# Optimization experiments

Hardware: AMD Instinct MI355X
Metric: run time of the kernel (lower is better)

Reference implementation:

```python
import jax, jax.numpy as jnp
import numpy as np

B, T, V, K = 4, 1024, 32000, 50000
EPS_T, EPS_M = 1e-8, 1e-12


def setup_inputs() -> dict:
    key = jax.random.key(0)
    k1, k2, k3, k4 = jax.random.split(key, 4)
    probs = jax.random.uniform(k1, (B, T, V), dtype=jnp.float32)
    # normalize so rows are valid distributions (faithful to softmax outputs)
    probs = probs / probs.sum(-1, keepdims=True)
    target_probs = jax.random.uniform(k2, (K,), dtype=jnp.float32) * (1.0 / K)
    target_oov = jax.random.uniform(k3, (1,), dtype=jnp.float32)
    mask = jnp.ones((B, T), dtype=bool)
    pairs = jax.random.randint(k4, (K, 2), 0, V, dtype=jnp.int64 if jax.config.jax_enable_x64 else jnp.int32)
    return {"probs": probs, "target_probs": target_probs, "target_oov": target_oov,
            "mask": mask, "pairs": pairs}


def reference(probs, target_probs, target_oov, mask, pairs):
    a = pairs[:, 0]  # (K,)
    b = pairs[:, 1]
    p_t = probs[:, :-1, :]   # (B, T-1, V)
    p_t1 = probs[:, 1:, :]
    pair_mask = (mask[:, :-1] & mask[:, 1:]).astype(jnp.float32)  # (B, T-1)
    # gather bigram probs: (B, T-1, K) joint, masked sum over batch/seq
    joint = p_t[..., a] * p_t1[..., b]
    topk_sum = jnp.einsum('btk,bt->k', joint, pair_mask)  # (K,)
    n_pairs = pair_mask.sum()

    # finalize
    n = jnp.maximum(n_pairs, 1.0)
    model_top = jnp.maximum(topk_sum / n, EPS_M)
    model_oov = jnp.clip(1.0 - model_top.sum(), EPS_M, 1.0 - EPS_T)
    tgt = jnp.maximum(target_probs, EPS_T)
    t_oov = jnp.maximum(target_oov[0], EPS_T)
    kl_top = (model_top * (jnp.log(model_top) - jnp.log(tgt))).sum()
    kl_oov = model_oov * (jnp.log(model_oov) - jnp.log(t_oov))
    return kl_top + kl_oov
```

## Files before the change

### kernel.cpp

```cpp
#include <hip/hip_runtime.h>
#include <stdint.h>

#define B_   4
#define T_   1024
#define V_   32000
#define K_   50000
#define N_   (B_*(T_-1))
#define TPB  1024
#define U_   49
#define KP   (TPB*U_)
#define POS_PER_BLK 16
#define G1   ((N_ + POS_PER_BLK - 1)/POS_PER_BLK)
#define EPSTGT 1e-8f
#define EPSMOD 1e-12f
#define MAXSLOTS 64

__device__ __forceinline__ uint32_t bf16rne(float x) {
    uint32_t u = __float_as_uint(x);
    u += 0x7FFFu + ((u >> 16) & 1u);
    return u >> 16;
}

__device__ __forceinline__ void stage_row(const float* __restrict__ probs, int r,
                                          ushort* dst, int tid) {
    const float4* src = (const float4*)(probs + (size_t)r * V_);
    for (int i = tid; i < V_ / 4; i += TPB) {
        float4 v = src[i];
        uint2 pk;
        pk.x = bf16rne(v.x) | (bf16rne(v.y) << 16);
        pk.y = bf16rne(v.z) | (bf16rne(v.w) << 16);
        *(uint2*)(dst + i * 4) = pk;
    }
}

__global__ void k_pack(const int* __restrict__ pairs, uint32_t* __restrict__ ppk) {
    int k = blockIdx.x * 256 + threadIdx.x;
    if (k >= KP) return;
    uint32_t v = 0;
    if (k < K_) {
        uint32_t a = (uint32_t)pairs[2 * k];
        uint32_t b = (uint32_t)pairs[2 * k + 1];
        v = ((a * 2u) << 16) | (b * 2u);
    }
    ppk[k] = v;
}

__global__ void k_mask(const unsigned char* __restrict__ mask, float* __restrict__ scalars) {
    __shared__ int red[16];
    int tid = threadIdx.x;
    int cnt = 0;
    for (int n = tid; n < N_; n += 1024) {
        int b = n / (T_ - 1);
        int t = n - b * (T_ - 1);
        int r = b * T_ + t;
        cnt += (mask[r] && mask[r + 1]) ? 1 : 0;
    }
    for (int off = 32; off > 0; off >>= 1) cnt += __shfl_down(cnt, off, 64);
    int wid = tid >> 6, lid = tid & 63;
    if (lid == 0) red[wid] = cnt;
    __syncthreads();
    if (tid == 0) {
        int s = 0;
        for (int w = 0; w < 16; ++w) s += red[w];
        scalars[0] = (float)s;
    }
}

__global__ __launch_bounds__(TPB) void k_main(
    const float* __restrict__ probs,
    const unsigned char* __restrict__ mask,
    const uint32_t* __restrict__ ppk,
    float* __restrict__ partials, int S)
{
    __shared__ __align__(16) ushort rows[2][V_];
    const int tid = threadIdx.x;
    const int g = blockIdx.x;
    const int n0 = g * POS_PER_BLK;
    const int n1 = min(N_, n0 + POS_PER_BLK);

    float acc[U_];
#pragma unroll
    for (int u = 0; u < U_; ++u) acc[u] = 0.f;

    int staged = -1;
    for (int n = n0; n < n1; ++n) {
        const int b = n / (T_ - 1);
        const int t = n - b * (T_ - 1);
        const int r0 = b * T_ + t;
        const int r1 = r0 + 1;

        __syncthreads();
        if (staged != r0) stage_row(probs, r0, rows[r0 & 1], tid);
        stage_row(probs, r1, rows[r1 & 1], tid);
        staged = r1;
        __syncthreads();

        if (!(mask[r0] && mask[r1])) continue;

        const ushort* rp = rows[r0 & 1];
        const ushort* rq = rows[r1 & 1];
        const uint32_t* pp = ppk + tid;
#pragma unroll
        for (int c = 0; c < U_; c += 7) {
            uint32_t pk[7];
#pragma unroll
            for (int j = 0; j < 7; ++j) pk[j] = pp[(c + j) * TPB];
#pragma unroll
            for (int j = 0; j < 7; ++j) {
                uint32_t ao = pk[j] >> 16;
                uint32_t bo = pk[j] & 0xFFFFu;
                ushort av = *(const ushort*)((const char*)rp + ao);
                ushort bv = *(const ushort*)((const char*)rq + bo);
                float af = __uint_as_float(((uint32_t)av) << 16);
                float bf = __uint_as_float(((uint32_t)bv) << 16);
                acc[c + j] = fmaf(af, bf, acc[c + j]);
            }
        }
    }

    float* slot = partials + (size_t)(g % S) * KP;
#pragma unroll
    for (int u = 0; u < U_; ++u)
        atomicAdd(slot + u * TPB + tid, acc[u]);
}

__global__ void k_reduce(const float* __restrict__ partials, const float* __restrict__ tgt,
                         float* __restrict__ scalars, int S) {
    int k = blockIdx.x * 256 + threadIdx.x;
    float n = fmaxf(scalars[0], 1.0f);
    float mt = 0.f, term = 0.f;
    if (k < K_) {
        float ts = 0.f;
        for (int s = 0; s < S; ++s) ts += partials[(size_t)s * KP + k];
        mt = fmaxf(ts / n, EPSMOD);
        float tg = fmaxf(tgt[k], EPSTGT);
        term = mt * (__logf(mt) - __logf(tg));
    }
    for (int off = 32; off > 0; off >>= 1) {
        mt += __shfl_down(mt, off, 64);
        term += __shfl_down(term, off, 64);
    }
    __shared__ float rm[4], rt[4];
    int wid = threadIdx.x >> 6, lid = threadIdx.x & 63;
    if (lid == 0) { rm[wid] = mt; rt[wid] = term; }
    __syncthreads();
    if (threadIdx.x == 0) {
        float sm = 0.f, st = 0.f;
        for (int w = 0; w < 4; ++w) { sm += rm[w]; st += rt[w]; }
        atomicAdd(&scalars[1], sm);
        atomicAdd(&scalars[2], st);
    }
}

__global__ void k_final(const float* __restrict__ scalars, const float* __restrict__ toov,
                        float* __restrict__ out) {
    float S1 = scalars[1], S2 = scalars[2];
    float moov = 1.f - S1;
    moov = fminf(fmaxf(moov, EPSMOD), 1.f - EPSTGT);
    float tv = fmaxf(toov[0], EPSTGT);
    out[0] = S2 + moov * (__logf(moov) - __logf(tv));
}

extern "C" void kernel_launch(void* const* d_in, const int* in_sizes, int n_in,
                              void* d_out, int out_size, void* d_ws, size_t ws_size,
                              hipStream_t stream) {
    const float* probs = (const float*)d_in[0];
    const float* tgt   = (const float*)d_in[1];
    const float* toov  = (const float*)d_in[2];
    const unsigned char* mask = (const unsigned char*)d_in[3];
    const int* pairs   = (const int*)d_in[4];
    float* out = (float*)d_out;

    char* ws = (char*)d_ws;
    uint32_t* ppk = (uint32_t*)ws;
    size_t off_sc = (size_t)KP * 4;
    float* scalars = (float*)(ws + off_sc);
    size_t off_pt = off_sc + 256;
    float* partials = (float*)(ws + off_pt);

    long avail = (long)ws_size - (long)off_pt;
    int S = (int)(avail / ((long)KP * 4));
    if (S > MAXSLOTS) S = MAXSLOTS;
    if (S < 1) S = 1;

    hipMemsetAsync(ws + off_sc, 0, 256 + (size_t)S * KP * 4, stream);
    k_pack<<<(KP + 255) / 256, 256, 0, stream>>>(pairs, ppk);
    k_mask<<<1, 1024, 0, stream>>>(mask, scalars);
    k_main<<<G1, TPB, 0, stream>>>(probs, mask, ppk, partials, S);
    k_reduce<<<(K_ + 255) / 256, 256, 0, stream>>>(partials, tgt, scalars, S);
    k_final<<<1, 1, 0, stream>>>(scalars, toov, out);
}
```

Before: 751.4 us.

## Prefetch next probability row into registers while computing current bigram gathers

Result: no change. 747.7 us (-0.5%).

```diff
diff --git a/kernel.cpp b/kernel.cpp
--- a/kernel.cpp
+++ b/kernel.cpp
@@ -14,22 +14,25 @@
 #define EPSTGT 1e-8f
 #define EPSMOD 1e-12f
 #define MAXSLOTS 64
+#define W4   (V_/4)
 
 __device__ __forceinline__ uint32_t bf16rne(float x) {
     uint32_t u = __float_as_uint(x);
     u += 0x7FFFu + ((u >> 16) & 1u);
     return u >> 16;
 }
+__device__ __forceinline__ uint2 pack4(float4 v) {
+    uint2 pk;
+    pk.x = bf16rne(v.x) | (bf16rne(v.y) << 16);
+    pk.y = bf16rne(v.z) | (bf16rne(v.w) << 16);
+    return pk;
+}
 
 __device__ __forceinline__ void stage_row(const float* __restrict__ probs, int r,
                                           ushort* dst, int tid) {
     const float4* src = (const float4*)(probs + (size_t)r * V_);
-    for (int i = tid; i < V_ / 4; i += TPB) {
-        float4 v = src[i];
-        uint2 pk;
-        pk.x = bf16rne(v.x) | (bf16rne(v.y) << 16);
-        pk.y = bf16rne(v.z) | (bf16rne(v.w) << 16);
-        *(uint2*)(dst + i * 4) = pk;
+    for (int i = tid; i < W4; i += TPB) {
+        *(uint2*)(dst + i * 4) = pack4(src[i]);
     }
 }
 
@@ -82,40 +85,98 @@
 #pragma unroll
     for (int u = 0; u < U_; ++u) acc[u] = 0.f;
 
-    int staged = -1;
+    int r0 = n0 + n0 / (T_ - 1);
+    int r1 = r0 + 1;
+    stage_row(probs, r0, rows[r0 & 1], tid);
+    stage_row(probs, r1, rows[r1 & 1], tid);
+
     for (int n = n0; n < n1; ++n) {
-        const int b = n / (T_ - 1);
-        const int t = n - b * (T_ - 1);
-        const int r0 = b * T_ + t;
-        const int r1 = r0 + 1;
+        const int nn = n + 1;
+        const bool more = (nn < n1);
+        const int nr0 = nn + nn / (T_ - 1);
+        const int nr1 = nr0 + 1;
+        const int pre_row = more ? ((nr0 == r1) ? nr1 : nr0) : -1;
+        const bool extra = more && (nr0 != r1);
+
+        const float4* src = (const float4*)(probs + (size_t)((pre_row >= 0) ? pre_row : 0) * V_);
+        float4 L0[4];
+#pragma unroll
+        for (int j = 0; j < 4; ++j) L0[j] = src[tid + j * TPB];
 
         __syncthreads();
-        if (staged != r0) stage_row(probs, r0, rows[r0 & 1], tid);
-        stage_row(probs, r1, rows[r1 & 1], tid);
-        staged = r1;
-        __syncthreads();
-
-        if (!(mask[r0] && mask[r1])) continue;
-
+
+        const bool active = mask[r0] && mask[r1];
         const ushort* rp = rows[r0 & 1];
         const ushort* rq = rows[r1 & 1];
         const uint32_t* pp = ppk + tid;
-#pragma unroll
-        for (int c = 0; c < U_; c += 7) {
-            uint32_t pk[7];
-#pragma unroll
-            for (int j = 0; j < 7; ++j) pk[j] = pp[(c + j) * TPB];
-#pragma unroll
-            for (int j = 0; j < 7; ++j) {
-                uint32_t ao = pk[j] >> 16;
-                uint32_t bo = pk[j] & 0xFFFFu;
-                ushort av = *(const ushort*)((const char*)rp + ao);
-                ushort bv = *(const ushort*)((const char*)rq + bo);
-                float af = __uint_as_float(((uint32_t)av) << 16);
-                float bf = __uint_as_float(((uint32_t)bv) << 16);
-                acc[c + j] = fmaf(af, bf, acc[c + j]);
-            }
-        }
+
+        if (active) {
+#pragma unroll
+            for (int c = 0; c < 28; c += 7) {
+                uint32_t pk[7];
+#pragma unroll
+                for (int j = 0; j < 7; ++j) pk[j] = pp[(c + j) * TPB];
+#pragma unroll
+                for (int j = 0; j < 7; ++j) {
+                    uint32_t ao = pk[j] >> 16;
+                    uint32_t bo = pk[j] & 0xFFFFu;
+                    ushort av = *(const ushort*)((const char*)rp + ao);
+                    ushort bv = *(const ushort*)((const char*)rq + bo);
+                    float af = __uint_as_float(((uint32_t)av) << 16);
+                    float bf = __uint_as_float(((uint32_t)bv) << 16);
+                    acc[c + j] = fmaf(af, bf, acc[c + j]);
+                }
+            }
+        }
+
+        uint2 P0[4];
+#pragma unroll
+        for (int j = 0; j < 4; ++j) P0[j] = pack4(L0[j]);
+        float4 L1[4];
+#pragma unroll
+        for (int j = 0; j < 4; ++j) {
+            int i = tid + (4 + j) * TPB;
+            int ic = (i < W4) ? i : 0;
+            L1[j] = src[ic];
+        }
+
+        if (active) {
+#pragma unroll
+            for (int c = 28; c < U_; c += 7) {
+                uint32_t pk[7];
+#pragma unroll
+                for (int j = 0; j < 7; ++j) pk[j] = pp[(c + j) * TPB];
+#pragma unroll
+                for (int j = 0; j < 7; ++j) {
+                    uint32_t ao = pk[j] >> 16;
+                    uint32_t bo = pk[j] & 0xFFFFu;
+                    ushort av = *(const ushort*)((const char*)rp + ao);
+                    ushort bv = *(const ushort*)((const char*)rq + bo);
+                    float af = __uint_as_float(((uint32_t)av) << 16);
+                    float bf = __uint_as_float(((uint32_t)bv) << 16);
+                    acc[c + j] = fmaf(af, bf, acc[c + j]);
+                }
+            }
+        }
+
+        __syncthreads();
+
+        if (pre_row >= 0) {
+            ushort* dst = rows[pre_row & 1];
+#pragma unroll
+            for (int j = 0; j < 4; ++j) {
+                int i = tid + j * TPB;
+                *(uint2*)(dst + i * 4) = P0[j];
+            }
+#pragma unroll
+            for (int j = 0; j < 4; ++j) {
+                int i = tid + (4 + j) * TPB;
+                if (i < W4) *(uint2*)(dst + i * 4) = pack4(L1[j]);
+            }
+            if (extra) stage_row(probs, nr1, rows[nr1 & 1], tid);
+        }
+
+        r0 = nr0; r1 = nr1;
     }
 
     float* slot = partials + (size_t)(g % S) * KP;
```
